# Kernel optimization log

Hardware: AMD Instinct MI355X
Metric: run time of the kernel (lower is better)

The kernel has to match this reference:

```python
import jax, jax.numpy as jnp
import numpy as np

# single species, e3tb basis 1s+1p+1d
FLIST = [1, 3, 5]           # flistnorbs (spin_factor = 1 pre-doubling)
NORB = 9                    # full_basis_norb
SPIN = 2                    # spin_deg -> block doubled
A, E, K = 192, 3072, 4
P = 58                      # sum_{i<=j} iorb*jorb = 1+3+5+9+15+25


def setup_inputs() -> dict:
    key = jax.random.key(0)
    ks = jax.random.split(key, 6)
    return dict(
        orbpair_hopping=jax.random.normal(ks[0], (E, P), jnp.float32),
        orbpair_onsite=jax.random.normal(ks[1], (A, P), jnp.float32),
        R_matrix=jax.random.normal(ks[2], (A, SPIN * NORB, SPIN * NORB), jnp.float32) * 0.1,
        kpoints=jax.random.uniform(ks[3], (K, 3), jnp.float32),
        edge_cell_shift=jax.random.normal(ks[4], (E, 3), jnp.float32),
        edge_index=jax.random.randint(ks[5], (2, E), 0, A, jnp.int64),
    )


def _assemble(feats):
    """Scatter flat orbpair features into upper-triangular [*, NORB, NORB] blocks."""
    n = feats.shape[0]
    H = jnp.zeros((n, NORB, NORB), feats.dtype)
    offs = np.concatenate([[0], np.cumsum(FLIST)])
    p = 0
    for i in range(len(FLIST)):
        for j in range(i, len(FLIST)):
            io, jo = FLIST[i], FLIST[j]
            f = 0.5 if i == j else 1.0  # diagonal orbpairs get 0.5 (hermitianized later)
            H = H.at[:, offs[i]:offs[i] + io, offs[j]:offs[j] + jo].set(
                f * feats[:, p:p + io * jo].reshape(n, io, jo))
            p += io * jo
    return H


def _spin_double(H):
    # H[:, :, 0, :, 0] = H[:, :, 1, :, 1] = H  (kron with eye(2), interleaved layout)
    n = H.shape[0]
    return jnp.einsum('aij,st->aisjt', H, jnp.eye(2, dtype=H.dtype)).reshape(n, SPIN * NORB, SPIN * NORB)


def reference(orbpair_hopping, orbpair_onsite, R_matrix, kpoints, edge_cell_shift, edge_index):
    s = SPIN * NORB
    src, dst = edge_index[0], edge_index[1]

    onsite = _spin_double(_assemble(orbpair_onsite))      # [A, s, s]
    hop = _spin_double(_assemble(orbpair_hopping))        # [E, s, s]

    # rotate: R @ H @ R^T (gathered per-edge for hoppings)
    onsite = jnp.einsum('aip,apq,ajq->aij', R_matrix, onsite, R_matrix)
    hop = jnp.einsum('eip,epq,ejq->eij', R_matrix[src], hop, R_matrix[dst])

    # Bloch phases exp(-2*pi*i k.S) per (k, edge)
    phase = jnp.exp(-2j * jnp.pi * (kpoints @ edge_cell_shift.T)).astype(jnp.complex64)  # [K, E]

    contrib = hop[None].astype(jnp.complex64) * phase[:, :, None, None]  # [K, E, s, s]
    pair = src * A + dst
    blk = jax.vmap(lambda c: jax.ops.segment_sum(c, pair, num_segments=A * A))(contrib)
    blk = blk.reshape(K, A, A, s, s)

    idx = jnp.arange(A)
    blk = blk.at[:, idx, idx].add(onsite[None].astype(jnp.complex64))  # onsite on diag, all k

    Hk = blk.transpose(0, 1, 3, 2, 4).reshape(K, A * s, A * s)
    return Hk + jnp.conj(jnp.swapaxes(Hk, 1, 2))
```

## Files before the change

### kernel.cpp

```cpp
#include <hip/hip_runtime.h>

#define PFEAT 58
#define S18   18
#define ENT   324
#define MAXE  128

__device__ __constant__ unsigned char c_row[PFEAT] = {
    0,0,0,0,0,0,0,0,0,
    1,1,1,2,2,2,3,3,3,
    1,1,1,1,1,2,2,2,2,2,3,3,3,3,3,
    4,4,4,4,4,5,5,5,5,5,6,6,6,6,6,7,7,7,7,7,8,8,8,8,8};
__device__ __constant__ unsigned char c_col[PFEAT] = {
    0,1,2,3,4,5,6,7,8,
    1,2,3,1,2,3,1,2,3,
    4,5,6,7,8,4,5,6,7,8,4,5,6,7,8,
    4,5,6,7,8,4,5,6,7,8,4,5,6,7,8,4,5,6,7,8,4,5,6,7,8};
__device__ __constant__ float c_fac[PFEAT] = {
    0.5f,1,1,1,1,1,1,1,1,
    0.5f,0.5f,0.5f,0.5f,0.5f,0.5f,0.5f,0.5f,0.5f,
    1,1,1,1,1,1,1,1,1,1,1,1,1,1,1,
    0.5f,0.5f,0.5f,0.5f,0.5f,0.5f,0.5f,0.5f,0.5f,0.5f,0.5f,0.5f,0.5f,
    0.5f,0.5f,0.5f,0.5f,0.5f,0.5f,0.5f,0.5f,0.5f,0.5f,0.5f,0.5f};

__device__ __forceinline__ bool detect_i64(const int* __restrict__ ei) {
    const uint2* p = (const uint2*)ei;
    unsigned acc = 0u;
#pragma unroll 8
    for (int m = 0; m < 64; ++m) acc |= p[m].y;
    return acc == 0u;
}

__device__ __forceinline__ int load_idx(const int* __restrict__ ei, int pos,
                                        bool is64, int A) {
    int v = is64 ? ei[2 * pos] : ei[pos];
    v = v < 0 ? 0 : (v >= A ? A - 1 : v);
    return v;
}

__device__ __forceinline__ void assemble_rotate(
    const float* __restrict__ feat, const float* __restrict__ Rs,
    const float* __restrict__ Rd, float* sH9, float* sRs, float* sRd,
    float* sT, float* sM, int t, int nthreads)
{
    for (int idx = t; idx < ENT; idx += nthreads) { sRs[idx] = Rs[idx]; sRd[idx] = Rd[idx]; }
    if (t < 81) sH9[t] = 0.f;
    __syncthreads();
    if (t < PFEAT) sH9[c_row[t] * 9 + c_col[t]] = c_fac[t] * feat[t];
    __syncthreads();

    for (int idx = t; idx < ENT; idx += nthreads) {
        const int pp = idx / S18, q = idx - pp * S18;
        const int i = pp >> 1, u = pp & 1;
        float acc = 0.f;
#pragma unroll
        for (int j = 0; j < 9; ++j)
            acc += sH9[i * 9 + j] * sRd[q * S18 + 2 * j + u];
        sT[idx] = acc;
    }
    __syncthreads();

    for (int idx = t; idx < ENT; idx += nthreads) {
        const int p = idx / S18, q = idx - p * S18;
        float acc = 0.f;
#pragma unroll
        for (int pp = 0; pp < S18; ++pp)
            acc += sRs[p * S18 + pp] * sT[pp * S18 + q];
        sM[idx] = acc;
    }
}


__global__ __launch_bounds__(256) void build_csr_kernel(
    const int* __restrict__ ei, int E, int A,
    int* __restrict__ offsets,
    int2* __restrict__ entries)
{
    extern __shared__ int smem[];
    int* scnt = smem;
    int* scur = smem + A;
    __shared__ int sflag;
    const int t = threadIdx.x;
    if (t == 0) sflag = detect_i64(ei) ? 1 : 0;
    for (int a = t; a < A; a += 256) scnt[a] = 0;
    __syncthreads();
    const bool s64 = sflag != 0;
    for (int e = t; e < E; e += 256) {
        const int a = load_idx(ei, e, s64, A);
        const int b = load_idx(ei, E + e, s64, A);
        atomicAdd(&scnt[a], 1);
        atomicAdd(&scnt[b], 1);
    }
    __syncthreads();
    if (t == 0) {
        int acc = 0;
        for (int a = 0; a < A; ++a) { scur[a] = acc; acc += scnt[a]; }
    }
    __syncthreads();
    for (int a = t; a < A; a += 256) offsets[a] = scur[a];
    if (t == 0) offsets[A] = scur[A - 1] + scnt[A - 1];
    __syncthreads();
    for (int e = t; e < E; e += 256) {
        const int a = load_idx(ei, e, s64, A);
        const int b = load_idx(ei, E + e, s64, A);
        const int p = atomicAdd(&scur[a], 1);
        entries[p] = make_int2(e, b);
        const int q = atomicAdd(&scur[b], 1);
        entries[q] = make_int2(e | (1 << 30), a);
    }
}

__global__ __launch_bounds__(256) void phase_kernel(
    const float* __restrict__ kpts, const float* __restrict__ shift,
    float* __restrict__ pcos, float* __restrict__ psin, int E, int K)
{
    const int idx = blockIdx.x * 256 + threadIdx.x;
    if (idx >= E * K) return;
    const int e = idx / K, k = idx - e * K;
    const float dot = kpts[k * 3 + 0] * shift[3 * e + 0]
                    + kpts[k * 3 + 1] * shift[3 * e + 1]
                    + kpts[k * 3 + 2] * shift[3 * e + 2];
    float sv, cv;
    sincosf(-6.28318530717958647692f * dot, &sv, &cv);
    pcos[idx] = cv;
    psin[idx] = sv;
}

__global__ __launch_bounds__(128) void rotate_kernel(
    const float* __restrict__ hop_feat, const float* __restrict__ ons_feat,
    const float* __restrict__ R, const int* __restrict__ ei,
    float* __restrict__ hop_rot, float* __restrict__ hop_rotT,
    float* __restrict__ ons_rot, int E, int A, int hasT)
{
    __shared__ float sH9[81];
    __shared__ float sRs[ENT];
    __shared__ float sRd[ENT];
    __shared__ float sT[ENT];
    __shared__ float sM[ENT];
    __shared__ int   sflag;

    const int item = blockIdx.x;
    const int t = threadIdx.x;
    if (t == 0) sflag = detect_i64(ei) ? 1 : 0;
    __syncthreads();
    const bool s64 = sflag != 0;

    const float* feat; const float* Rs; const float* Rd; float* outp;
    if (item < E) {
        const int a_s = load_idx(ei, item, s64, A);
        const int a_d = load_idx(ei, E + item, s64, A);
        feat = hop_feat + (size_t)item * PFEAT;
        Rs = R + (size_t)a_s * ENT;
        Rd = R + (size_t)a_d * ENT;
        outp = hop_rot + (size_t)item * ENT;
    } else {
        const int a = item - E;
        feat = ons_feat + (size_t)a * PFEAT;
        Rs = R + (size_t)a * ENT;
        Rd = Rs;
        outp = ons_rot + (size_t)a * ENT;
    }

    assemble_rotate(feat, Rs, Rd, sH9, sRs, sRd, sT, sM, t, 128);
    __syncthreads();

    for (int idx = t; idx < ENT; idx += 128) outp[idx] = sM[idx];
    if (item < E && hasT) {
        float* outpT = hop_rotT + (size_t)item * ENT;
        for (int idx = t; idx < ENT; idx += 128) {
            const int p = idx / S18, q = idx - p * S18;
            outpT[idx] = sM[q * S18 + p];
        }
    }
}

__global__ __launch_bounds__(256) void write_kernel(
    const float* __restrict__ hop_rot,
    const float* __restrict__ hop_rotT,
    const float* __restrict__ ons_rot,
    const int*   __restrict__ offsets,
    const int2*  __restrict__ entries,
    const float* __restrict__ pcos,
    const float* __restrict__ psin,
    float* __restrict__ outf,
    int A, int K, int cplx, int hasT, long long lim)
{
    extern __shared__ float rowbuf[];
    __shared__ int2  sent[MAXE];
    __shared__ float sphc[MAXE];
    __shared__ float sphs[MAXE];

    const int N = A * S18;
    const int I = blockIdx.x;
    const int k = blockIdx.y;
    const int t = threadIdx.x;
    const int a = I / S18, i = I - a * S18;
    const int stride = cplx ? 2 : 1;
    const int nbuf = stride * N;

    for (int idx = t; idx < nbuf; idx += 256) rowbuf[idx] = 0.f;

    const int beg = offsets[a], end = offsets[a + 1];
    const int cnt = end - beg;
    const int nst = cnt < MAXE ? cnt : MAXE;
    for (int n = t; n < nst; n += 256) {
        const int2 ent = entries[beg + n];
        sent[n] = ent;
        const int e0 = ent.x & 0x3FFFFFFF;
        sphc[n] = pcos[e0 * K + k];
        if (cplx) sphs[n] = psin[e0 * K + k];
    }
    __syncthreads();

    if (t < S18) {
        const float v = ons_rot[a * ENT + i * S18 + t] + ons_rot[a * ENT + t * S18 + i];
        atomicAdd(&rowbuf[stride * (a * S18 + t)], v);
    }

    const int total = cnt * S18;
    for (int m = t; m < total; m += 256) {
        const int n = m / S18, l = m - n * S18;
        int2 ent; float pc, ps = 0.f;
        if (n < MAXE) {
            ent = sent[n]; pc = sphc[n]; if (cplx) ps = sphs[n];
        } else {
            ent = entries[beg + n];
            const int e0 = ent.x & 0x3FFFFFFF;
            pc = pcos[e0 * K + k]; if (cplx) ps = psin[e0 * K + k];
        }
        const int conjf = (ent.x >> 30) & 1;
        const int e = ent.x & 0x3FFFFFFF;
        const int b = ent.y;
        float v;
        if (!conjf)     v = hop_rot [(size_t)e * ENT + i * S18 + l];
        else if (hasT)  v = hop_rotT[(size_t)e * ENT + i * S18 + l];
        else            v = hop_rot [(size_t)e * ENT + l * S18 + i];
        atomicAdd(&rowbuf[stride * (b * S18 + l)], v * pc);
        if (cplx)
            atomicAdd(&rowbuf[stride * (b * S18 + l) + 1], conjf ? -v * ps : v * ps);
    }
    __syncthreads();

    const long long base = (long long)stride * ((long long)k * N + I) * (long long)N;
    float* dst = outf + base;
    if (base + nbuf <= lim && (nbuf & 3) == 0) {
        const float4* s4 = (const float4*)rowbuf;
        float4* d4 = (float4*)dst;
        const int nv = nbuf >> 2;
        for (int idx = t; idx < nv; idx += 256) d4[idx] = s4[idx];
    } else {
        for (int idx = t; idx < nbuf; idx += 256)
            if (base + idx < lim) dst[idx] = rowbuf[idx];
    }
}


__global__ __launch_bounds__(256) void zero_kernel(float* __restrict__ p, long long n)
{
    const long long i4 = ((long long)blockIdx.x * 256 + threadIdx.x) * 4;
    if (i4 + 3 < n) {
        *(float4*)(p + i4) = make_float4(0.f, 0.f, 0.f, 0.f);
    } else if (i4 < n) {
        for (long long i = i4; i < n; ++i) p[i] = 0.f;
    }
}

__global__ __launch_bounds__(256) void edge_kernel(
    const float* __restrict__ hop_feat, const float* __restrict__ R,
    const float* __restrict__ kpts, const float* __restrict__ shift,
    const int* __restrict__ edge_index, float* __restrict__ outf,
    int E, int A, int K, int cplx, long long lim)
{
    __shared__ float sH9[81];
    __shared__ float sRs[ENT];
    __shared__ float sRd[ENT];
    __shared__ float sT[ENT];
    __shared__ float sM[ENT];
    __shared__ float sC[8];
    __shared__ float sS[8];

    const int e = blockIdx.x;
    const int t = threadIdx.x;
    const int N = A * S18;
    const long long N2 = (long long)N * N;

    const bool is64 = detect_i64(edge_index);
    const int a = load_idx(edge_index, e, is64, A);
    const int b = load_idx(edge_index, E + e, is64, A);

    if (t < K && t < 8) {
        const float sx = shift[e * 3 + 0], sy = shift[e * 3 + 1], sz = shift[e * 3 + 2];
        const float dot = kpts[t * 3 + 0] * sx + kpts[t * 3 + 1] * sy + kpts[t * 3 + 2] * sz;
        float sv, cv;
        sincosf(-6.28318530717958647692f * dot, &sv, &cv);
        sC[t] = cv; sS[t] = sv;
    }

    assemble_rotate(hop_feat + (size_t)e * PFEAT,
                    R + (size_t)a * ENT, R + (size_t)b * ENT,
                    sH9, sRs, sRd, sT, sM, t, 256);
    __syncthreads();

    const int total = K * ENT;
    for (int idx = t; idx < total; idx += 256) {
        const int k = idx / ENT, r = idx - k * ENT;
        const int i = r / S18, j = r - i * S18;
        const float v = sM[r];
        const float re = v * sC[k];
        const float im = v * sS[k];
        const long long I = (long long)a * S18 + i;
        const long long J = (long long)b * S18 + j;
        const long long p1 = k * N2 + I * N + J;
        const long long p2 = k * N2 + J * N + I;
        if (cplx) {
            if (2 * p1 + 1 < lim) { atomicAdd(&outf[2 * p1], re); atomicAdd(&outf[2 * p1 + 1], im); }
            if (2 * p2 + 1 < lim) { atomicAdd(&outf[2 * p2], re); atomicAdd(&outf[2 * p2 + 1], -im); }
        } else {
            if (p1 < lim) atomicAdd(&outf[p1], re);
            if (p2 < lim) atomicAdd(&outf[p2], re);
        }
    }
}

__global__ __launch_bounds__(128) void onsite_kernel(
    const float* __restrict__ ons_feat, const float* __restrict__ R,
    float* __restrict__ outf, int A, int K, int cplx, long long lim)
{
    __shared__ float sH9[81];
    __shared__ float sRs[ENT];
    __shared__ float sRd[ENT];
    __shared__ float sT[ENT];
    __shared__ float sM[ENT];

    const int a = blockIdx.x;
    const int t = threadIdx.x;
    const int N = A * S18;
    const long long N2 = (long long)N * N;

    assemble_rotate(ons_feat + (size_t)a * PFEAT,
                    R + (size_t)a * ENT, R + (size_t)a * ENT,
                    sH9, sRs, sRd, sT, sM, t, 128);
    __syncthreads();

    for (int idx = t; idx < ENT; idx += 128) {
        const int i = idx / S18, j = idx - (idx / S18) * S18;
        const float v = sM[i * S18 + j] + sM[j * S18 + i];
        const long long I = (long long)a * S18 + i;
        const long long J = (long long)a * S18 + j;
        for (int k = 0; k < K; ++k) {
            const long long p1 = k * N2 + I * N + J;
            const long long off = cplx ? 2 * p1 : p1;
            if (off < lim) outf[off] += v;
        }
    }
}

extern "C" void kernel_launch(void* const* d_in, const int* in_sizes, int n_in,
                              void* d_out, int out_size, void* d_ws, size_t ws_size,
                              hipStream_t stream) {
    const float* hop_feat   = (const float*)d_in[0];
    const float* ons_feat   = (const float*)d_in[1];
    const float* R          = (const float*)d_in[2];
    const float* kpts       = (const float*)d_in[3];
    const float* shift      = (const float*)d_in[4];
    const int*   edge_index = (const int*)d_in[5];

    const int E = in_sizes[0] / PFEAT;
    const int A = in_sizes[1] / PFEAT;
    const int K = in_sizes[3] / 3;

    const long long N  = (long long)A * S18;
    const long long n_real = (long long)K * N * N;
    const long long lim = (long long)out_size;
    const int cplx = (lim >= 2 * n_real) ? 1 : 0;

    float* outf = (float*)d_out;

    char* ws = (char*)d_ws;
    const size_t off_hop = 0;
    const size_t off_ons = off_hop + (size_t)E * ENT * 4;
    const size_t off_ent = off_ons + (size_t)A * ENT * 4;
    const size_t off_off = off_ent + (size_t)2 * E * 8;
    const size_t off_pc  = off_off + (size_t)(A + 2) * 4;
    const size_t off_ps  = off_pc  + (size_t)E * K * 4;
    const size_t base_need = off_ps + (size_t)E * K * 4;
    const size_t off_hT  = base_need;
    const size_t full_need = off_hT + (size_t)E * ENT * 4;

    if (ws_size >= base_need && A <= 4096) {
        const int hasT = (ws_size >= full_need) ? 1 : 0;
        float* hop_rot  = (float*)(ws + off_hop);
        float* ons_rot  = (float*)(ws + off_ons);
        int2*  entries  = (int2*)(ws + off_ent);
        int*   offsets  = (int*)(ws + off_off);
        float* pcos     = (float*)(ws + off_pc);
        float* psin     = (float*)(ws + off_ps);
        float* hop_rotT = (float*)(ws + off_hT);

        build_csr_kernel<<<1, 256, 2 * A * sizeof(int), stream>>>(edge_index, E, A,
                                                                  offsets, entries);
        phase_kernel<<<(E * K + 255) / 256, 256, 0, stream>>>(kpts, shift, pcos, psin, E, K);
        rotate_kernel<<<E + A, 128, 0, stream>>>(hop_feat, ons_feat, R, edge_index,
                                                 hop_rot, hop_rotT, ons_rot, E, A, hasT);
        const size_t shmem = (size_t)(cplx ? 2 : 1) * N * sizeof(float);
        dim3 grid((unsigned)N, (unsigned)K);
        write_kernel<<<grid, 256, shmem, stream>>>(hop_rot, hop_rotT, ons_rot,
                                                   offsets, entries, pcos, psin,
                                                   outf, A, K, cplx, hasT, lim);
    } else {
        const long long n4 = (lim + 3) / 4;
        const int zgrid = (int)((n4 + 255) / 256);
        zero_kernel<<<zgrid, 256, 0, stream>>>(outf, lim);
        edge_kernel<<<E, 256, 0, stream>>>(hop_feat, R, kpts, shift, edge_index,
                                           outf, E, A, K, cplx, lim);
        onsite_kernel<<<A, 128, 0, stream>>>(ons_feat, R, outf, A, K, cplx, lim);
    }
}
```

Measured before the change: 258.6 us.

## Process nine output rows per write block and fold phase computation into rotate kernel

The write kernel now launches one block per atom half (nine rows) instead of one block per output row. This reuses the staged CSR entries, phases and onsite block across nine rows and cuts the grid from A*18 to A*2 blocks per k-point. The separate phase kernel is removed and its sincos work is done inside the rotate kernel's edge blocks, saving one launch. In exchange there is less block-level parallelism and extra barriers per row. The fast path now also requires an even atom count.

```diff
diff --git a/kernel.cpp b/kernel.cpp
--- a/kernel.cpp
+++ b/kernel.cpp
@@ -109,27 +109,13 @@
     }
 }
 
-__global__ __launch_bounds__(256) void phase_kernel(
-    const float* __restrict__ kpts, const float* __restrict__ shift,
-    float* __restrict__ pcos, float* __restrict__ psin, int E, int K)
-{
-    const int idx = blockIdx.x * 256 + threadIdx.x;
-    if (idx >= E * K) return;
-    const int e = idx / K, k = idx - e * K;
-    const float dot = kpts[k * 3 + 0] * shift[3 * e + 0]
-                    + kpts[k * 3 + 1] * shift[3 * e + 1]
-                    + kpts[k * 3 + 2] * shift[3 * e + 2];
-    float sv, cv;
-    sincosf(-6.28318530717958647692f * dot, &sv, &cv);
-    pcos[idx] = cv;
-    psin[idx] = sv;
-}
-
 __global__ __launch_bounds__(128) void rotate_kernel(
     const float* __restrict__ hop_feat, const float* __restrict__ ons_feat,
     const float* __restrict__ R, const int* __restrict__ ei,
+    const float* __restrict__ kpts, const float* __restrict__ shift,
     float* __restrict__ hop_rot, float* __restrict__ hop_rotT,
-    float* __restrict__ ons_rot, int E, int A, int hasT)
+    float* __restrict__ ons_rot, float* __restrict__ pcos,
+    float* __restrict__ psin, int E, int A, int K, int hasT)
 {
     __shared__ float sH9[81];
     __shared__ float sRs[ENT];
@@ -152,6 +138,15 @@
         Rs = R + (size_t)a_s * ENT;
         Rd = R + (size_t)a_d * ENT;
         outp = hop_rot + (size_t)item * ENT;
+        for (int k = t; k < K; k += 128) {
+            const float dot = kpts[k * 3 + 0] * shift[3 * item + 0]
+                            + kpts[k * 3 + 1] * shift[3 * item + 1]
+                            + kpts[k * 3 + 2] * shift[3 * item + 2];
+            float sv, cv;
+            sincosf(-6.28318530717958647692f * dot, &sv, &cv);
+            pcos[item * K + k] = cv;
+            psin[item * K + k] = sv;
+        }
     } else {
         const int a = item - E;
         feat = ons_feat + (size_t)a * PFEAT;
@@ -188,16 +183,17 @@
     __shared__ int2  sent[MAXE];
     __shared__ float sphc[MAXE];
     __shared__ float sphs[MAXE];
+    __shared__ float sons[ENT];
 
     const int N = A * S18;
-    const int I = blockIdx.x;
+    const int a    = blockIdx.x >> 1;
+    const int half = blockIdx.x & 1;
     const int k = blockIdx.y;
     const int t = threadIdx.x;
-    const int a = I / S18, i = I - a * S18;
+    const int i0 = half * 9;
     const int stride = cplx ? 2 : 1;
     const int nbuf = stride * N;
-
-    for (int idx = t; idx < nbuf; idx += 256) rowbuf[idx] = 0.f;
+    const int nbuf4 = nbuf >> 2;
 
     const int beg = offsets[a], end = offsets[a + 1];
     const int cnt = end - beg;
@@ -209,47 +205,57 @@
         sphc[n] = pcos[e0 * K + k];
         if (cplx) sphs[n] = psin[e0 * K + k];
     }
-    __syncthreads();
-
-    if (t < S18) {
-        const float v = ons_rot[a * ENT + i * S18 + t] + ons_rot[a * ENT + t * S18 + i];
-        atomicAdd(&rowbuf[stride * (a * S18 + t)], v);
-    }
-
+    for (int idx = t; idx < ENT; idx += 256) sons[idx] = ons_rot[a * ENT + idx];
+    __syncthreads();
+
+    float4* rb4 = (float4*)rowbuf;
     const int total = cnt * S18;
-    for (int m = t; m < total; m += 256) {
-        const int n = m / S18, l = m - n * S18;
-        int2 ent; float pc, ps = 0.f;
-        if (n < MAXE) {
-            ent = sent[n]; pc = sphc[n]; if (cplx) ps = sphs[n];
+
+    for (int ri = 0; ri < 9; ++ri) {
+        const int i = i0 + ri;
+        for (int idx = t; idx < nbuf4; idx += 256)
+            rb4[idx] = make_float4(0.f, 0.f, 0.f, 0.f);
+        __syncthreads();
+
+        if (t < S18)
+            atomicAdd(&rowbuf[stride * (a * S18 + t)],
+                      sons[i * S18 + t] + sons[t * S18 + i]);
+
+        for (int m = t; m < total; m += 256) {
+            const int n = m / S18, l = m - n * S18;
+            int2 ent; float pc, ps = 0.f;
+            if (n < MAXE) {
+                ent = sent[n]; pc = sphc[n]; if (cplx) ps = sphs[n];
+            } else {
+                ent = entries[beg + n];
+                const int e0 = ent.x & 0x3FFFFFFF;
+                pc = pcos[e0 * K + k]; if (cplx) ps = psin[e0 * K + k];
+            }
+            const int conjf = (ent.x >> 30) & 1;
+            const int e = ent.x & 0x3FFFFFFF;
+            const int b = ent.y;
+            float v;
+            if (!conjf)     v = hop_rot [(size_t)e * ENT + i * S18 + l];
+            else if (hasT)  v = hop_rotT[(size_t)e * ENT + i * S18 + l];
+            else            v = hop_rot [(size_t)e * ENT + l * S18 + i];
+            atomicAdd(&rowbuf[stride * (b * S18 + l)], v * pc);
+            if (cplx)
+                atomicAdd(&rowbuf[stride * (b * S18 + l) + 1], conjf ? -v * ps : v * ps);
+        }
+        __syncthreads();
+
+        const long long base = (long long)stride
+                             * ((long long)k * N + (long long)a * S18 + i)
+                             * (long long)N;
+        float* dst = outf + base;
+        if (base + nbuf <= lim && ((base & 3) == 0)) {
+            float4* d4 = (float4*)dst;
+            for (int idx = t; idx < nbuf4; idx += 256) d4[idx] = rb4[idx];
         } else {
-            ent = entries[beg + n];
-            const int e0 = ent.x & 0x3FFFFFFF;
-            pc = pcos[e0 * K + k]; if (cplx) ps = psin[e0 * K + k];
-        }
-        const int conjf = (ent.x >> 30) & 1;
-        const int e = ent.x & 0x3FFFFFFF;
-        const int b = ent.y;
-        float v;
-        if (!conjf)     v = hop_rot [(size_t)e * ENT + i * S18 + l];
-        else if (hasT)  v = hop_rotT[(size_t)e * ENT + i * S18 + l];
-        else            v = hop_rot [(size_t)e * ENT + l * S18 + i];
-        atomicAdd(&rowbuf[stride * (b * S18 + l)], v * pc);
-        if (cplx)
-            atomicAdd(&rowbuf[stride * (b * S18 + l) + 1], conjf ? -v * ps : v * ps);
-    }
-    __syncthreads();
-
-    const long long base = (long long)stride * ((long long)k * N + I) * (long long)N;
-    float* dst = outf + base;
-    if (base + nbuf <= lim && (nbuf & 3) == 0) {
-        const float4* s4 = (const float4*)rowbuf;
-        float4* d4 = (float4*)dst;
-        const int nv = nbuf >> 2;
-        for (int idx = t; idx < nv; idx += 256) d4[idx] = s4[idx];
-    } else {
-        for (int idx = t; idx < nbuf; idx += 256)
-            if (base + idx < lim) dst[idx] = rowbuf[idx];
+            for (int idx = t; idx < nbuf; idx += 256)
+                if (base + idx < lim) dst[idx] = rowbuf[idx];
+        }
+        __syncthreads();
     }
 }
 
@@ -386,7 +392,7 @@
     const size_t off_hT  = base_need;
     const size_t full_need = off_hT + (size_t)E * ENT * 4;
 
-    if (ws_size >= base_need && A <= 4096) {
+    if (ws_size >= base_need && A <= 4096 && (A & 1) == 0) {
         const int hasT = (ws_size >= full_need) ? 1 : 0;
         float* hop_rot  = (float*)(ws + off_hop);
         float* ons_rot  = (float*)(ws + off_ons);
@@ -398,11 +404,11 @@
 
         build_csr_kernel<<<1, 256, 2 * A * sizeof(int), stream>>>(edge_index, E, A,
                                                                   offsets, entries);
-        phase_kernel<<<(E * K + 255) / 256, 256, 0, stream>>>(kpts, shift, pcos, psin, E, K);
         rotate_kernel<<<E + A, 128, 0, stream>>>(hop_feat, ons_feat, R, edge_index,
-                                                 hop_rot, hop_rotT, ons_rot, E, A, hasT);
+                                                 kpts, shift, hop_rot, hop_rotT,
+                                                 ons_rot, pcos, psin, E, A, K, hasT);
         const size_t shmem = (size_t)(cplx ? 2 : 1) * N * sizeof(float);
-        dim3 grid((unsigned)N, (unsigned)K);
+        dim3 grid((unsigned)(A * 2), (unsigned)K);
         write_kernel<<<grid, 256, shmem, stream>>>(hop_rot, hop_rotT, ons_rot,
                                                    offsets, entries, pcos, psin,
                                                    outf, A, K, cplx, hasT, lim);
```

After: 262.6 us. No clear change (+1.6%).
